# Performance work log

Hardware: AMD Instinct MI355X
Metric: run time of the kernel (lower is better)

## Reference

```python
import jax, jax.numpy as jnp
import numpy as np

D = 768      # embedding_dim
H = 12       # num_heads
HS = D // H  # head_size = 64
B, T, TC = 8, 1024, 256
FF = 4 * D
EPS = 1e-5


def _layernorm(x, w, b):
    mu = jnp.mean(x, axis=-1, keepdims=True)
    var = jnp.mean((x - mu) ** 2, axis=-1, keepdims=True)
    return (x - mu) / jnp.sqrt(var + EPS) * w + b


def _mha(x_q, x_kv, Wq, bq, Wk, bk, Wv, bv):
    # Batched equivalent of the per-head Python loop: weights stacked as [H, D, HS].
    q = jnp.einsum('btd,hde->bhte', x_q, Wq) + bq[None, :, None, :]
    k = jnp.einsum('bsd,hde->bhse', x_kv, Wk) + bk[None, :, None, :]
    v = jnp.einsum('bsd,hde->bhse', x_kv, Wv) + bv[None, :, None, :]
    scale = HS ** (-0.5)  # original scales by C**-0.5 with C = head_size
    wei = jax.nn.softmax(jnp.einsum('bhte,bhse->bhts', q, k) * scale, axis=-1)
    o = jnp.einsum('bhts,bhse->bhte', wei, v)  # [B,H,T,HS]
    # torch.cat over heads on dim=-1 == transpose then merge head dims
    return o.transpose(0, 2, 1, 3).reshape(o.shape[0], o.shape[2], H * HS)


def setup_inputs() -> dict:
    key = jax.random.key(0)
    ks = jax.random.split(key, 20)
    s = 0.02
    inp = {
        'img_embedding': jax.random.normal(ks[0], (B, T, D), jnp.float32),
        'context': jax.random.normal(ks[1], (B, TC, D), jnp.float32),
        'ln1_w': jnp.ones((D,), jnp.float32), 'ln1_b': jnp.zeros((D,), jnp.float32),
        'sWq': jax.random.normal(ks[2], (H, D, HS), jnp.float32) * s,
        'sbq': jnp.zeros((H, HS), jnp.float32),
        'sWk': jax.random.normal(ks[3], (H, D, HS), jnp.float32) * s,
        'sbk': jnp.zeros((H, HS), jnp.float32),
        'sWv': jax.random.normal(ks[4], (H, D, HS), jnp.float32) * s,
        'sbv': jnp.zeros((H, HS), jnp.float32),
        'ln2_w': jnp.ones((D,), jnp.float32), 'ln2_b': jnp.zeros((D,), jnp.float32),
        'cWq': jax.random.normal(ks[5], (H, D, HS), jnp.float32) * s,
        'cbq': jnp.zeros((H, HS), jnp.float32),
        'cWk': jax.random.normal(ks[6], (H, D, HS), jnp.float32) * s,
        'cbk': jnp.zeros((H, HS), jnp.float32),
        'cWv': jax.random.normal(ks[7], (H, D, HS), jnp.float32) * s,
        'cbv': jnp.zeros((H, HS), jnp.float32),
        'ln3_w': jnp.ones((D,), jnp.float32), 'ln3_b': jnp.zeros((D,), jnp.float32),
        'W1': jax.random.normal(ks[8], (D, FF), jnp.float32) * s,
        'b1': jnp.zeros((FF,), jnp.float32),
        'W2': jax.random.normal(ks[9], (FF, D), jnp.float32) * s,
        'b2': jnp.zeros((D,), jnp.float32),
    }
    return inp


def reference(img_embedding, context, ln1_w, ln1_b, sWq, sbq, sWk, sbk, sWv, sbv,
              ln2_w, ln2_b, cWq, cbq, cWk, cbk, cWv, cbv, ln3_w, ln3_b,
              W1, b1, W2, b2):
    x = img_embedding
    x = x + _mha(_layernorm(x, ln1_w, ln1_b), _layernorm(x, ln1_w, ln1_b),
                 sWq, sbq, sWk, sbk, sWv, sbv)
    x = x + _mha(_layernorm(x, ln2_w, ln2_b), context,
                 cWq, cbq, cWk, cbk, cWv, cbv)
    h = _layernorm(x, ln3_w, ln3_b)
    ff = jax.nn.silu(h @ W1 + b1) @ W2 + b2
    return x + ff
```

## Files before the change

kernel.cpp:

```cpp
#include <hip/hip_runtime.h>
#include <hip/hip_bf16.h>


#define D_EMB 768
#define N_HEADS 12
#define HEAD 64
#define B_SZ 8
#define T_IMG 1024
#define T_CTX 256
#define FF_DIM 3072
#define ROWS_IMG (B_SZ * T_IMG)
#define ROWS_CTX (B_SZ * T_CTX)
#define BIGCOL (1 << 28)
#define PART_STRIDE (ROWS_IMG * D_EMB)

typedef __bf16 bf16x8 __attribute__((ext_vector_type(8)));
typedef __bf16 bf16x4 __attribute__((ext_vector_type(4)));
typedef float f32x4 __attribute__((ext_vector_type(4)));

__device__ __forceinline__ void gld16(const void* g, void* l) {
    __builtin_amdgcn_global_load_lds(
        (const __attribute__((address_space(1))) unsigned int*)g,
        (__attribute__((address_space(3))) unsigned int*)l, 16, 0, 0);
}

__global__ __launch_bounds__(256) void copy4_kernel(const float4* __restrict__ src,
                                                    float4* __restrict__ dst) {
    int i = blockIdx.x * 256 + threadIdx.x;
    dst[i] = src[i];
}

__global__ __launch_bounds__(256) void cvt_bf16_kernel(const float* __restrict__ src,
                                                       __bf16* __restrict__ dst, int n4) {
    int i = blockIdx.x * 256 + threadIdx.x;
    if (i >= n4) return;
    float4 v = ((const float4*)src)[i];
    __bf16* d = dst + i * 4;
    d[0] = (__bf16)v.x; d[1] = (__bf16)v.y; d[2] = (__bf16)v.z; d[3] = (__bf16)v.w;
}

__global__ __launch_bounds__(256) void reduce_w2_kernel(
    const __bf16* __restrict__ P, const float* __restrict__ b2,
    float* __restrict__ X) {
    int i = blockIdx.x * 256 + threadIdx.x;
    int base = i * 4;
    int col = base % D_EMB;
    bf16x4 p0 = *(const bf16x4*)&P[base];
    bf16x4 p1 = *(const bf16x4*)&P[PART_STRIDE + base];
    float4 x = *(float4*)&X[base];
    float4 bb = *(const float4*)&b2[col];
    x.x += (float)p0[0] + (float)p1[0] + bb.x;
    x.y += (float)p0[1] + (float)p1[1] + bb.y;
    x.z += (float)p0[2] + (float)p1[2] + bb.z;
    x.w += (float)p0[3] + (float)p1[3] + bb.w;
    *(float4*)&X[base] = x;
}

__global__ __launch_bounds__(256) void transpose_cvt_kernel(
    const float* __restrict__ src, __bf16* __restrict__ dst,
    int src_rows, int src_cols) {
    __shared__ float tile[64][65];
    int tid = threadIdx.x;
    int r0 = blockIdx.y * 64, c0 = blockIdx.x * 64;
    int lr = tid >> 4, lc = (tid & 15) * 4;
#pragma unroll
    for (int i = 0; i < 4; i++) {
        float4 v = *(const float4*)&src[(size_t)(r0 + i * 16 + lr) * src_cols + c0 + lc];
        tile[i * 16 + lr][lc] = v.x; tile[i * 16 + lr][lc + 1] = v.y;
        tile[i * 16 + lr][lc + 2] = v.z; tile[i * 16 + lr][lc + 3] = v.w;
    }
    __syncthreads();
#pragma unroll
    for (int i = 0; i < 4; i++) {
        int cc = i * 16 + lr;
        int rr = (tid & 15) * 4;
        bf16x4 o;
#pragma unroll
        for (int j = 0; j < 4; j++) o[j] = (__bf16)tile[rr + j][cc];
        *(bf16x4*)&dst[(size_t)(c0 + cc) * src_rows + r0 + rr] = o;
    }
}

__global__ __launch_bounds__(256) void repack_qkv_t_kernel(
    const float* __restrict__ Wq, const float* __restrict__ Wk, const float* __restrict__ Wv,
    const float* __restrict__ bq, const float* __restrict__ bk, const float* __restrict__ bv,
    __bf16* __restrict__ Wt, float* __restrict__ bp) {
    __shared__ float tile[64][65];
    int tid = threadIdx.x;
    int which = blockIdx.y / 12, h = blockIdx.y - which * 12;
    int d0 = blockIdx.x * 64;
    const float* W = (which == 0) ? Wq : ((which == 1) ? Wk : Wv);
    const float* src = W + ((size_t)h * D_EMB + d0) * HEAD;
    int lr = tid >> 4, lc = (tid & 15) * 4;
#pragma unroll
    for (int i = 0; i < 4; i++) {
        float4 v = *(const float4*)&src[(size_t)(i * 16 + lr) * HEAD + lc];
        tile[i * 16 + lr][lc] = v.x; tile[i * 16 + lr][lc + 1] = v.y;
        tile[i * 16 + lr][lc + 2] = v.z; tile[i * 16 + lr][lc + 3] = v.w;
    }
    __syncthreads();
#pragma unroll
    for (int i = 0; i < 4; i++) {
        int e = i * 16 + lr;
        int dd = (tid & 15) * 4;
        bf16x4 o;
#pragma unroll
        for (int j = 0; j < 4; j++) o[j] = (__bf16)tile[dd + j][e];
        *(bf16x4*)&Wt[(size_t)(which * 768 + h * 64 + e) * D_EMB + d0 + dd] = o;
    }
    if (blockIdx.x == 0 && tid < 64) {
        const float* bb = (which == 0) ? bq : ((which == 1) ? bk : bv);
        bp[which * 768 + h * 64 + tid] = bb[h * 64 + tid];
    }
}

__global__ __launch_bounds__(256) void ln_kernel(const float* __restrict__ x,
                                                 const float* __restrict__ lw,
                                                 const float* __restrict__ lb,
                                                 __bf16* __restrict__ y) {
    int row = blockIdx.x;
    int tid = threadIdx.x;
    const float* xr = x + (size_t)row * D_EMB;
    float a0 = xr[tid], a1 = xr[tid + 256], a2 = xr[tid + 512];
    float s = a0 + a1 + a2;
    float ss = a0 * a0 + a1 * a1 + a2 * a2;
#pragma unroll
    for (int off = 32; off > 0; off >>= 1) {
        s += __shfl_down(s, off, 64);
        ss += __shfl_down(ss, off, 64);
    }
    __shared__ float red[8];
    __shared__ float stats[2];
    int wv = tid >> 6, lane = tid & 63;
    if (lane == 0) { red[wv] = s; red[4 + wv] = ss; }
    __syncthreads();
    if (tid == 0) {
        float S = red[0] + red[1] + red[2] + red[3];
        float SS = red[4] + red[5] + red[6] + red[7];
        float mu = S * (1.0f / D_EMB);
        float var = SS * (1.0f / D_EMB) - mu * mu;
        stats[0] = mu;
        stats[1] = rsqrtf(var + 1e-5f);
    }
    __syncthreads();
    float mu = stats[0], rs = stats[1];
    __bf16* yr = y + (size_t)row * D_EMB;
    yr[tid]       = (__bf16)((a0 - mu) * rs * lw[tid]       + lb[tid]);
    yr[tid + 256] = (__bf16)((a1 - mu) * rs * lw[tid + 256] + lb[tid + 256]);
    yr[tid + 512] = (__bf16)((a2 - mu) * rs * lw[tid + 512] + lb[tid + 512]);
}

__global__ __launch_bounds__(256) void mfma_gemm_bt(
    const __bf16* __restrict__ A, int lda,
    const __bf16* __restrict__ Bt, int ldb,
    const float* __restrict__ bias,
    __bf16* __restrict__ Cb, int ldc,
    int Kc, int act, int qlimit,
    __bf16* __restrict__ VTout, int vtok, int vcol0, int kcol0, int kcol1) {
    __shared__ __bf16 As[128 * 32];
    __shared__ __bf16 Bs[128 * 32];
    int tid = threadIdx.x;
    int bx = blockIdx.x, by = blockIdx.y, kz = blockIdx.z;
    int w = tid >> 6, lane = tid & 63;
    int c = lane & 15, quad = lane >> 4;
    int wm = (w >> 1) * 64, wn = (w & 1) * 64;

    f32x4 acc[4][4];
#pragma unroll
    for (int i = 0; i < 4; i++)
#pragma unroll
        for (int j = 0; j < 4; j++) acc[i][j] = (f32x4){0.f, 0.f, 0.f, 0.f};

    int srow = tid >> 2;
    int scol = (tid & 3) * 8;
    const __bf16* Ag = A + (size_t)(by * 128 + srow) * lda + (size_t)kz * Kc + scol;
    const __bf16* Bg = Bt + (size_t)(bx * 128 + srow) * ldb + (size_t)kz * Kc + scol;
    char* AsB = (char*)As + w * 1024;
    char* BsB = (char*)Bs + w * 1024;

    for (int k0 = 0; k0 < Kc; k0 += 32) {
        gld16(Ag + k0, AsB);
        gld16(Ag + (size_t)64 * lda + k0, AsB + 4096);
        gld16(Bg + k0, BsB);
        gld16(Bg + (size_t)64 * ldb + k0, BsB + 4096);
        __syncthreads();
        bf16x8 af[4], bfr[4];
#pragma unroll
        for (int mi = 0; mi < 4; mi++)
            af[mi] = *(const bf16x8*)&As[(wm + mi * 16 + c) * 32 + quad * 8];
#pragma unroll
        for (int ni = 0; ni < 4; ni++)
            bfr[ni] = *(const bf16x8*)&Bs[(wn + ni * 16 + c) * 32 + quad * 8];
#pragma unroll
        for (int mi = 0; mi < 4; mi++)
#pragma unroll
            for (int ni = 0; ni < 4; ni++)
                acc[mi][ni] = __builtin_amdgcn_mfma_f32_16x16x32_bf16(
                    bfr[ni], af[mi], acc[mi][ni], 0, 0, 0);
        __syncthreads();
    }

#pragma unroll
    for (int mi = 0; mi < 4; mi++) {
#pragma unroll
        for (int ni = 0; ni < 4; ni++) {
            int row = by * 128 + wm + mi * 16 + c;
            int colbase = bx * 128 + wn + ni * 16 + quad * 4;
            float bvv[4] = {0.f, 0.f, 0.f, 0.f};
            if (bias && kz == 0) {
                float4 b4 = *(const float4*)&bias[colbase];
                bvv[0] = b4.x; bvv[1] = b4.y; bvv[2] = b4.z; bvv[3] = b4.w;
            }
            float qs = (colbase < qlimit) ? 0.125f : 1.0f;
            float v[4];
#pragma unroll
            for (int r = 0; r < 4; r++) {
                float t = (acc[mi][ni][r] + bvv[r]) * qs;
                if (act == 1) t = t / (1.0f + __expf(-t));
                v[r] = t;
            }
            if (VTout && colbase >= vcol0) {
                int hc = colbase - vcol0;
                int hh = hc >> 6, ebase = hc & 63;
                int tok = row;
#pragma unroll
                for (int r = 0; r < 4; r++) {
                    int e = ebase + r;
                    int sl = ((((tok >> 3) & 7) ^ (e & 7)) << 3) | (tok & 7);
                    VTout[(size_t)(hh * 64 + e) * vtok + (tok & ~63) + sl] = (__bf16)v[r];
                }
            } else if (colbase >= kcol0 && colbase < kcol1) {
                int hc = colbase - kcol0;
                int hh = hc >> 6, ebase = hc & 63;
                int tok = row;
                int es = (((ebase >> 3) ^ (tok & 7)) << 3) | (ebase & 7);
                bf16x4 pv;
#pragma unroll
                for (int r = 0; r < 4; r++) pv[r] = (__bf16)v[r];
                *(bf16x4*)&Cb[(size_t)tok * ldc + kcol0 + hh * 64 + es] = pv;
            } else {
                __bf16* dst = Cb + (size_t)kz * PART_STRIDE;
                bf16x4 pv;
#pragma unroll
                for (int r = 0; r < 4; r++) pv[r] = (__bf16)v[r];
                *(bf16x4*)&dst[(size_t)row * ldc + colbase] = pv;
            }
        }
    }
}

__device__ __forceinline__ void stage_half(const __bf16* __restrict__ G, int ld,
                                           int kcol, __bf16* lds_half, int tid) {
    int w = tid >> 6;
#pragma unroll
    for (int j = 0; j < 2; j++) {
        int oe = (j * 512 + tid) * 8;
        int r = oe >> 6;
        int colx = (oe & 63) ^ ((r & 7) << 3);
        gld16(G + (size_t)r * ld + kcol + colx,
              (char*)lds_half + (j * 512 + w * 64) * 16);
    }
}

__device__ __forceinline__ bf16x8 lds_frag(const __bf16* h, int row, int kk, int quad) {
    int off = (kk * 32 + quad * 8) ^ ((row & 7) << 3);
    return *(const bf16x8*)&h[row * 64 + off];
}

template <int MG, int KK>
__device__ __forceinline__ void gemm_phase(
    const __bf16* Ah, const __bf16* Bh, int rBbase, int c, int quad,
    f32x4 (&acc)[8][4],
    bool dostage, const __bf16* Gs, int ldg, int kcol, __bf16* ldsdst, int tid) {
    bf16x8 af[4], bfr[4];
#pragma unroll
    for (int mi = 0; mi < 4; mi++)
        af[mi] = lds_frag(Ah, MG * 64 + mi * 16 + c, KK, quad);
#pragma unroll
    for (int ni = 0; ni < 4; ni++)
        bfr[ni] = lds_frag(Bh, rBbase + ni * 16 + c, KK, quad);
    if (dostage) stage_half(Gs, ldg, kcol, ldsdst, tid);
    __builtin_amdgcn_s_barrier();
    asm volatile("s_waitcnt lgkmcnt(0)" ::: "memory");
    __builtin_amdgcn_s_setprio(1);
#pragma unroll
    for (int mi = 0; mi < 4; mi++)
#pragma unroll
        for (int ni = 0; ni < 4; ni++)
            acc[MG * 4 + mi][ni] = __builtin_amdgcn_mfma_f32_16x16x32_bf16(
                bfr[ni], af[mi], acc[MG * 4 + mi][ni], 0, 0, 0);
    __builtin_amdgcn_s_setprio(0);
    __builtin_amdgcn_s_barrier();
}

__global__ __launch_bounds__(512, 2) void mfma_gemm_bt256(
    const __bf16* __restrict__ A, int lda,
    const __bf16* __restrict__ Bt, int ldb,
    const float* __restrict__ bias,
    __bf16* __restrict__ Cb, int ldc,
    int Kc, int act, int qlimit,
    __bf16* __restrict__ VTout, int vtok, int vcol0, int kcol0, int kcol1) {
    __shared__ __bf16 SM[8 * 8192];
    int tid = threadIdx.x;
    int bx = blockIdx.x, by = blockIdx.y, kz = blockIdx.z;
    int w = tid >> 6, lane = tid & 63, c = lane & 15, quad = lane >> 4;
    int wr = w >> 2, wc = w & 3;

    const __bf16* Ag0 = A + (size_t)(by * 256) * lda + (size_t)kz * Kc;
    const __bf16* Ag1 = Ag0 + (size_t)128 * lda;
    const __bf16* Bg0 = Bt + (size_t)(bx * 256) * ldb + (size_t)kz * Kc;
    const __bf16* Bg1 = Bg0 + (size_t)128 * ldb;

    f32x4 acc[8][4];
#pragma unroll
    for (int i = 0; i < 8; i++)
#pragma unroll
        for (int j = 0; j < 4; j++) acc[i][j] = (f32x4){0.f, 0.f, 0.f, 0.f};

    stage_half(Ag0, lda, 0, SM + 0 * 8192, tid);
    stage_half(Ag1, lda, 0, SM + 1 * 8192, tid);
    stage_half(Bg0, ldb, 0, SM + 2 * 8192, tid);
    stage_half(Bg1, ldb, 0, SM + 3 * 8192, tid);

    int nt = Kc >> 6;
    for (int t = 0; t < nt; t++) {
        int cur = (t & 1) << 2;
        int nxt = cur ^ 4;
        bool pf = (t + 1) < nt;
        int kc1 = (t + 1) << 6;
        if (pf) {
            stage_half(Ag0, lda, kc1, SM + (nxt + 0) * 8192, tid);
            asm volatile("s_waitcnt vmcnt(2)" ::: "memory");
        } else {
            asm volatile("s_waitcnt vmcnt(0)" ::: "memory");
        }
        __builtin_amdgcn_s_barrier();

        const __bf16* Ah = SM + (cur + wr) * 8192;
        const __bf16* Bh = SM + (cur + 2 + (wc >> 1)) * 8192;
        int rBbase = (wc & 1) * 64;
        gemm_phase<0, 0>(Ah, Bh, rBbase, c, quad, acc, pf, Ag1, lda, kc1, SM + (nxt + 1) * 8192, tid);
        gemm_phase<0, 1>(Ah, Bh, rBbase, c, quad, acc, pf, Bg0, ldb, kc1, SM + (nxt + 2) * 8192, tid);
        gemm_phase<1, 0>(Ah, Bh, rBbase, c, quad, acc, pf, Bg1, ldb, kc1, SM + (nxt + 3) * 8192, tid);
        gemm_phase<1, 1>(Ah, Bh, rBbase, c, quad, acc, false, Ag0, lda, 0, SM, tid);
    }

#pragma unroll
    for (int mi = 0; mi < 8; mi++) {
        int row = by * 256 + wr * 128 + (mi >> 2) * 64 + (mi & 3) * 16 + c;
#pragma unroll
        for (int ni = 0; ni < 4; ni++) {
            int colbase = bx * 256 + wc * 64 + ni * 16 + quad * 4;
            float bvv[4] = {0.f, 0.f, 0.f, 0.f};
            if (bias && kz == 0) {
                float4 b4 = *(const float4*)&bias[colbase];
                bvv[0] = b4.x; bvv[1] = b4.y; bvv[2] = b4.z; bvv[3] = b4.w;
            }
            float qs = (colbase < qlimit) ? 0.125f : 1.0f;
            float v[4];
#pragma unroll
            for (int r = 0; r < 4; r++) {
                float tv = (acc[mi][ni][r] + bvv[r]) * qs;
                if (act == 1) tv = tv / (1.0f + __expf(-tv));
                v[r] = tv;
            }
            if (VTout && colbase >= vcol0) {
                int hc = colbase - vcol0;
                int hh = hc >> 6, ebase = hc & 63;
                int tok = row;
#pragma unroll
                for (int r = 0; r < 4; r++) {
                    int e = ebase + r;
                    int sl = ((((tok >> 3) & 7) ^ (e & 7)) << 3) | (tok & 7);
                    VTout[(size_t)(hh * 64 + e) * vtok + (tok & ~63) + sl] = (__bf16)v[r];
                }
            } else if (colbase >= kcol0 && colbase < kcol1) {
                int hc = colbase - kcol0;
                int hh = hc >> 6, ebase = hc & 63;
                int tok = row;
                int es = (((ebase >> 3) ^ (tok & 7)) << 3) | (ebase & 7);
                bf16x4 pv;
#pragma unroll
                for (int r = 0; r < 4; r++) pv[r] = (__bf16)v[r];
                *(bf16x4*)&Cb[(size_t)tok * ldc + kcol0 + hh * 64 + es] = pv;
            } else {
                __bf16* dst = Cb + (size_t)kz * PART_STRIDE;
                bf16x4 pv;
#pragma unroll
                for (int r = 0; r < 4; r++) pv[r] = (__bf16)v[r];
                *(bf16x4*)&dst[(size_t)row * ldc + colbase] = pv;
            }
        }
    }
}

__global__ __launch_bounds__(128, 2) void mfma_attn(
    const __bf16* __restrict__ Q, int qld,
    const __bf16* __restrict__ Kp, int kld,
    const __bf16* __restrict__ VTg, int vtok,
    int kv_tokens, float* __restrict__ X) {
    __shared__ __bf16 Kt[64 * 64];
    __shared__ __bf16 VT[80 * 64];
    __shared__ __bf16 Ps[128 * 76];
    int tid = threadIdx.x;
    int qt = blockIdx.x & 7;
    int bh = blockIdx.x >> 3;
    int b = bh / N_HEADS, h = bh - b * N_HEADS;
    int w = tid >> 6, lane = tid & 63, c = lane & 15, quad = lane >> 4;
    int q0 = qt * 128;

    for (int i = tid; i < 16 * 64; i += 128)
        VT[64 * 64 + i] = (i < 64) ? (__bf16)1.0f : (__bf16)0.0f;

    {
        const __bf16* Qg = Q + (size_t)(b * T_IMG + q0 + (tid >> 3)) * qld
                           + h * HEAD + (tid & 7) * 8;
        char* QsB = (char*)Ps + w * 1024;
#pragma unroll
        for (int j = 0; j < 8; j++)
            gld16(Qg + (size_t)j * 16 * qld, QsB + j * 2048);
    }
    __syncthreads();
    bf16x8 qa[4][2];
#pragma unroll
    for (int st = 0; st < 4; st++)
#pragma unroll
        for (int ch = 0; ch < 2; ch++)
            qa[st][ch] = *(const bf16x8*)&Ps[(w * 64 + st * 16 + c) * 64 + ch * 32 + quad * 8];
    __syncthreads();

    f32x4 o[4][5];
#pragma unroll
    for (int st = 0; st < 4; st++)
#pragma unroll
        for (int ut = 0; ut < 5; ut++) o[st][ut] = (f32x4){0.f, 0.f, 0.f, 0.f};

    char* KtB = (char*)Kt + w * 1024;
    char* VtB = (char*)VT + w * 1024;
    int ntiles = kv_tokens >> 6;
    for (int t = 0; t < ntiles; t++) {
        const __bf16* Kg = Kp + (size_t)(b * kv_tokens + t * 64 + (tid >> 3)) * kld
                           + h * HEAD + (tid & 7) * 8;
        const __bf16* Vg = VTg + (size_t)(h * HEAD + (tid >> 3)) * vtok
                           + b * kv_tokens + t * 64 + (tid & 7) * 8;
#pragma unroll
        for (int j = 0; j < 4; j++) {
            gld16(Kg + (size_t)j * 16 * kld, KtB + j * 2048);
            gld16(Vg + (size_t)j * 16 * vtok, VtB + j * 2048);
        }
        __syncthreads();

        bf16x8 kb[4][2];
#pragma unroll
        for (int nt = 0; nt < 4; nt++)
#pragma unroll
            for (int ch = 0; ch < 2; ch++)
                kb[nt][ch] = *(const bf16x8*)&Kt[(nt * 16 + c) * 64
                                + (((ch * 4 + quad) ^ (c & 7)) << 3)];
#pragma unroll
        for (int st = 0; st < 4; st++) {
            f32x4 s[4];
#pragma unroll
            for (int nt = 0; nt < 4; nt++) {
                s[nt] = (f32x4){0.f, 0.f, 0.f, 0.f};
                s[nt] = __builtin_amdgcn_mfma_f32_16x16x32_bf16(kb[nt][0], qa[st][0], s[nt], 0, 0, 0);
                s[nt] = __builtin_amdgcn_mfma_f32_16x16x32_bf16(kb[nt][1], qa[st][1], s[nt], 0, 0, 0);
            }
#pragma unroll
            for (int nt = 0; nt < 4; nt++) {
                bf16x4 pk;
#pragma unroll
                for (int r = 0; r < 4; r++) pk[r] = (__bf16)__expf(s[nt][r]);
                *(bf16x4*)&Ps[(size_t)(w * 64 + st * 16 + c) * 76 + nt * 16 + quad * 4] = pk;
            }
        }
        __syncthreads();

        bf16x8 vb[5][2];
#pragma unroll
        for (int ut = 0; ut < 5; ut++)
#pragma unroll
            for (int ch = 0; ch < 2; ch++)
                vb[ut][ch] = *(const bf16x8*)&VT[(ut * 16 + c) * 64
                                + (((ch * 4 + quad) ^ (c & 7)) << 3)];
#pragma unroll
        for (int st = 0; st < 4; st++) {
            bf16x8 pa0 = *(const bf16x8*)&Ps[(w * 64 + st * 16 + c) * 76 + quad * 8];
            bf16x8 pa1 = *(const bf16x8*)&Ps[(w * 64 + st * 16 + c) * 76 + 32 + quad * 8];
#pragma unroll
            for (int ut = 0; ut < 5; ut++) {
                o[st][ut] = __builtin_amdgcn_mfma_f32_16x16x32_bf16(pa0, vb[ut][0], o[st][ut], 0, 0, 0);
                o[st][ut] = __builtin_amdgcn_mfma_f32_16x16x32_bf16(pa1, vb[ut][1], o[st][ut], 0, 0, 0);
            }
        }
        __syncthreads();
    }

#pragma unroll
    for (int st = 0; st < 4; st++) {
        float lr[4];
#pragma unroll
        for (int r = 0; r < 4; r++) lr[r] = __shfl(o[st][4][r], lane & 48, 64);
#pragma unroll
        for (int ut = 0; ut < 4; ut++) {
#pragma unroll
            for (int r = 0; r < 4; r++) {
                int row = b * T_IMG + q0 + w * 64 + st * 16 + quad * 4 + r;
                int col = h * HEAD + ut * 16 + c;
                X[(size_t)row * D_EMB + col] += o[st][ut][r] / lr[r];
            }
        }
    }
}

extern "C" void kernel_launch(void* const* d_in, const int* in_sizes, int n_in,
                              void* d_out, int out_size, void* d_ws, size_t ws_size,
                              hipStream_t stream) {
    const float* img  = (const float*)d_in[0];
    const float* ctx  = (const float*)d_in[1];
    const float* ln1w = (const float*)d_in[2];  const float* ln1b = (const float*)d_in[3];
    const float* sWq  = (const float*)d_in[4];  const float* sbq  = (const float*)d_in[5];
    const float* sWk  = (const float*)d_in[6];  const float* sbk  = (const float*)d_in[7];
    const float* sWv  = (const float*)d_in[8];  const float* sbv  = (const float*)d_in[9];
    const float* ln2w = (const float*)d_in[10]; const float* ln2b = (const float*)d_in[11];
    const float* cWq  = (const float*)d_in[12]; const float* cbq  = (const float*)d_in[13];
    const float* cWk  = (const float*)d_in[14]; const float* cbk  = (const float*)d_in[15];
    const float* cWv  = (const float*)d_in[16]; const float* cbv  = (const float*)d_in[17];
    const float* ln3w = (const float*)d_in[18]; const float* ln3b = (const float*)d_in[19];
    const float* W1   = (const float*)d_in[20]; const float* b1   = (const float*)d_in[21];
    const float* W2   = (const float*)d_in[22]; const float* b2   = (const float*)d_in[23];

    float* X = (float*)d_out;

    char* p = (char*)d_ws;
    __bf16* LNb  = (__bf16*)p; p += (size_t)ROWS_IMG * D_EMB * 2;
    __bf16* VTg  = (__bf16*)p; p += (size_t)12 * 64 * ROWS_IMG * 2;
    __bf16* BIG  = (__bf16*)p; p += (size_t)ROWS_IMG * FF_DIM * 2;
    __bf16* ctxb = (__bf16*)p; p += (size_t)ROWS_CTX * D_EMB * 2;
    __bf16* Wt   = (__bf16*)p; p += (size_t)2304 * 768 * 2;
    __bf16* cWt  = (__bf16*)p; p += (size_t)2304 * 768 * 2;
    __bf16* W1t  = (__bf16*)p; p += (size_t)FF_DIM * 768 * 2;
    __bf16* W2t  = (__bf16*)p; p += (size_t)768 * FF_DIM * 2;
    __bf16* VTc  = (__bf16*)p; p += (size_t)12 * 64 * ROWS_CTX * 2;
    float*  bp   = (float*)p;  p += 2304 * 4;
    float*  cbp  = (float*)p;  p += 2304 * 4;
    __bf16* Pk   = LNb;
    __bf16* QKVb = BIG;
    __bf16* Qc   = BIG;
    __bf16* KVc  = BIG + (size_t)ROWS_IMG * 768;
    __bf16* FFh  = BIG;

    copy4_kernel<<<ROWS_IMG * D_EMB / 4 / 256, 256, 0, stream>>>(
        (const float4*)img, (float4*)X);
    cvt_bf16_kernel<<<(ROWS_CTX * D_EMB / 4 + 255) / 256, 256, 0, stream>>>(
        ctx, ctxb, ROWS_CTX * D_EMB / 4);
    repack_qkv_t_kernel<<<dim3(12, 36), 256, 0, stream>>>(
        sWq, sWk, sWv, sbq, sbk, sbv, Wt, bp);
    repack_qkv_t_kernel<<<dim3(12, 36), 256, 0, stream>>>(
        cWq, cWk, cWv, cbq, cbk, cbv, cWt, cbp);
    transpose_cvt_kernel<<<dim3(FF_DIM / 64, 768 / 64), 256, 0, stream>>>(
        W1, W1t, 768, FF_DIM);
    transpose_cvt_kernel<<<dim3(768 / 64, FF_DIM / 64), 256, 0, stream>>>(
        W2, W2t, FF_DIM, 768);

    ln_kernel<<<ROWS_IMG, 256, 0, stream>>>(X, ln1w, ln1b, LNb);
    mfma_gemm_bt256<<<dim3(2304 / 256, ROWS_IMG / 256), 512, 0, stream>>>(
        LNb, D_EMB, Wt, D_EMB, bp, QKVb, 2304, D_EMB, 0, 768,
        VTg, ROWS_IMG, 1536, 768, 1536);
    mfma_attn<<<96 * 8, 128, 0, stream>>>(
        QKVb, 2304, QKVb + 768, 2304, VTg, ROWS_IMG, T_IMG, X);

    ln_kernel<<<ROWS_IMG, 256, 0, stream>>>(X, ln2w, ln2b, LNb);
    mfma_gemm_bt<<<dim3(768 / 128, ROWS_IMG / 128), 256, 0, stream>>>(
        LNb, D_EMB, cWt, D_EMB, cbp, Qc, 768, D_EMB, 0, 768,
        nullptr, 0, BIGCOL, BIGCOL, BIGCOL);
    mfma_gemm_bt<<<dim3(1536 / 128, ROWS_CTX / 128), 256, 0, stream>>>(
        ctxb, D_EMB, cWt + (size_t)768 * 768, D_EMB, cbp + 768,
        KVc, 1536, D_EMB, 0, 0,
        VTc, ROWS_CTX, 768, 0, 768);
    mfma_attn<<<96 * 8, 128, 0, stream>>>(
        Qc, 768, KVc, 1536, VTc, ROWS_CTX, T_CTX, X);

    ln_kernel<<<ROWS_IMG, 256, 0, stream>>>(X, ln3w, ln3b, LNb);
    mfma_gemm_bt256<<<dim3(FF_DIM / 256, ROWS_IMG / 256), 512, 0, stream>>>(
        LNb, D_EMB, W1t, D_EMB, b1, FFh, FF_DIM, D_EMB, 1, 0,
        nullptr, 0, BIGCOL, BIGCOL, BIGCOL);
    mfma_gemm_bt256<<<dim3(768 / 256, ROWS_IMG / 256, 2), 512, 0, stream>>>(
        FFh, FF_DIM, W2t, FF_DIM, nullptr, Pk, D_EMB, 1536, 0, 0,
        nullptr, 0, BIGCOL, BIGCOL, BIGCOL);
    reduce_w2_kernel<<<ROWS_IMG * D_EMB / 4 / 256, 256, 0, stream>>>(Pk, b2, X);
}
```

Measured before the change: 531.6 us.

## Prefetch GEMM tiles two stages ahead and swizzle workgroup order

```diff
diff --git a/kernel.cpp b/kernel.cpp
--- a/kernel.cpp
+++ b/kernel.cpp
@@ -267,32 +267,6 @@
     return *(const bf16x8*)&h[row * 64 + off];
 }
 
-template <int MG, int KK>
-__device__ __forceinline__ void gemm_phase(
-    const __bf16* Ah, const __bf16* Bh, int rBbase, int c, int quad,
-    f32x4 (&acc)[8][4],
-    bool dostage, const __bf16* Gs, int ldg, int kcol, __bf16* ldsdst, int tid) {
-    bf16x8 af[4], bfr[4];
-#pragma unroll
-    for (int mi = 0; mi < 4; mi++)
-        af[mi] = lds_frag(Ah, MG * 64 + mi * 16 + c, KK, quad);
-#pragma unroll
-    for (int ni = 0; ni < 4; ni++)
-        bfr[ni] = lds_frag(Bh, rBbase + ni * 16 + c, KK, quad);
-    if (dostage) stage_half(Gs, ldg, kcol, ldsdst, tid);
-    __builtin_amdgcn_s_barrier();
-    asm volatile("s_waitcnt lgkmcnt(0)" ::: "memory");
-    __builtin_amdgcn_s_setprio(1);
-#pragma unroll
-    for (int mi = 0; mi < 4; mi++)
-#pragma unroll
-        for (int ni = 0; ni < 4; ni++)
-            acc[MG * 4 + mi][ni] = __builtin_amdgcn_mfma_f32_16x16x32_bf16(
-                bfr[ni], af[mi], acc[MG * 4 + mi][ni], 0, 0, 0);
-    __builtin_amdgcn_s_setprio(0);
-    __builtin_amdgcn_s_barrier();
-}
-
 __global__ __launch_bounds__(512, 2) void mfma_gemm_bt256(
     const __bf16* __restrict__ A, int lda,
     const __bf16* __restrict__ Bt, int ldb,
@@ -302,9 +276,16 @@
     __bf16* __restrict__ VTout, int vtok, int vcol0, int kcol0, int kcol1) {
     __shared__ __bf16 SM[8 * 8192];
     int tid = threadIdx.x;
-    int bx = blockIdx.x, by = blockIdx.y, kz = blockIdx.z;
+    int kz = blockIdx.z;
+    int gx = gridDim.x;
+    int nwg = gx * gridDim.y;
+    int orig = blockIdx.y * gx + blockIdx.x;
+    int swz = (orig & 7) * (nwg >> 3) + (orig >> 3);
+    int bx = swz % gx, by = swz / gx;
+
     int w = tid >> 6, lane = tid & 63, c = lane & 15, quad = lane >> 4;
     int wr = w >> 2, wc = w & 3;
+    int rBbase = (wc & 1) * 64;
 
     const __bf16* Ag0 = A + (size_t)(by * 256) * lda + (size_t)kz * Kc;
     const __bf16* Ag1 = Ag0 + (size_t)128 * lda;
@@ -321,28 +302,54 @@
     stage_half(Ag1, lda, 0, SM + 1 * 8192, tid);
     stage_half(Bg0, ldb, 0, SM + 2 * 8192, tid);
     stage_half(Bg1, ldb, 0, SM + 3 * 8192, tid);
+    stage_half(Ag0, lda, 64, SM + 4 * 8192, tid);
+    stage_half(Ag1, lda, 64, SM + 5 * 8192, tid);
+    stage_half(Bg0, ldb, 64, SM + 6 * 8192, tid);
+    stage_half(Bg1, ldb, 64, SM + 7 * 8192, tid);
+    asm volatile("s_waitcnt vmcnt(8)" ::: "memory");
+    __builtin_amdgcn_s_barrier();
 
     int nt = Kc >> 6;
     for (int t = 0; t < nt; t++) {
         int cur = (t & 1) << 2;
-        int nxt = cur ^ 4;
-        bool pf = (t + 1) < nt;
-        int kc1 = (t + 1) << 6;
-        if (pf) {
-            stage_half(Ag0, lda, kc1, SM + (nxt + 0) * 8192, tid);
-            asm volatile("s_waitcnt vmcnt(2)" ::: "memory");
-        } else {
-            asm volatile("s_waitcnt vmcnt(0)" ::: "memory");
-        }
-        __builtin_amdgcn_s_barrier();
-
         const __bf16* Ah = SM + (cur + wr) * 8192;
         const __bf16* Bh = SM + (cur + 2 + (wc >> 1)) * 8192;
-        int rBbase = (wc & 1) * 64;
-        gemm_phase<0, 0>(Ah, Bh, rBbase, c, quad, acc, pf, Ag1, lda, kc1, SM + (nxt + 1) * 8192, tid);
-        gemm_phase<0, 1>(Ah, Bh, rBbase, c, quad, acc, pf, Bg0, ldb, kc1, SM + (nxt + 2) * 8192, tid);
-        gemm_phase<1, 0>(Ah, Bh, rBbase, c, quad, acc, pf, Bg1, ldb, kc1, SM + (nxt + 3) * 8192, tid);
-        gemm_phase<1, 1>(Ah, Bh, rBbase, c, quad, acc, false, Ag0, lda, 0, SM, tid);
+#pragma unroll
+        for (int kk = 0; kk < 2; kk++) {
+            bf16x8 bfr[4];
+#pragma unroll
+            for (int ni = 0; ni < 4; ni++)
+                bfr[ni] = lds_frag(Bh, rBbase + ni * 16 + c, kk, quad);
+#pragma unroll
+            for (int mg = 0; mg < 2; mg++) {
+                bf16x8 af[4];
+#pragma unroll
+                for (int mi = 0; mi < 4; mi++)
+                    af[mi] = lds_frag(Ah, mg * 64 + mi * 16 + c, kk, quad);
+                __builtin_amdgcn_s_setprio(1);
+#pragma unroll
+                for (int mi = 0; mi < 4; mi++)
+#pragma unroll
+                    for (int ni = 0; ni < 4; ni++)
+                        acc[mg * 4 + mi][ni] = __builtin_amdgcn_mfma_f32_16x16x32_bf16(
+                            bfr[ni], af[mi], acc[mg * 4 + mi][ni], 0, 0, 0);
+                __builtin_amdgcn_s_setprio(0);
+            }
+        }
+        if (t + 1 < nt) {
+            __builtin_amdgcn_s_barrier();
+            if (t + 2 < nt) {
+                int kc = (t + 2) << 6;
+                stage_half(Ag0, lda, kc, SM + (cur + 0) * 8192, tid);
+                stage_half(Ag1, lda, kc, SM + (cur + 1) * 8192, tid);
+                stage_half(Bg0, ldb, kc, SM + (cur + 2) * 8192, tid);
+                stage_half(Bg1, ldb, kc, SM + (cur + 3) * 8192, tid);
+                asm volatile("s_waitcnt vmcnt(8)" ::: "memory");
+            } else {
+                asm volatile("s_waitcnt vmcnt(0)" ::: "memory");
+            }
+            __builtin_amdgcn_s_barrier();
+        }
     }
 
 #pragma unroll
```

New measurement: 511.8 us. -3.7%, faster.
